# Optimization experiments

Hardware: AMD Instinct MI355X
Metric: run time of the kernel (lower is better)

Reference implementation:

```python
import jax, jax.numpy as jnp
import numpy as np

B, S, H, U = 32, 2048, 1024, 1024


def setup_inputs() -> dict:
    key = jax.random.key(0)
    ks = jax.random.split(key, 5)
    sc = 1.0 / np.sqrt(H)
    return {
        "hidden_t": jax.random.normal(ks[0], (B, H), jnp.float32),
        "hiddens": jax.random.normal(ks[1], (B, S, H), jnp.float32),
        "W1": jax.random.normal(ks[2], (H, U), jnp.float32) * sc,
        "b1": jnp.zeros((U,), jnp.float32),
        "W2": jax.random.normal(ks[3], (H, U), jnp.float32) * sc,
        "b2": jnp.zeros((U,), jnp.float32),
        "V": jax.random.normal(ks[4], (U, 1), jnp.float32) * sc,
        "bV": jnp.zeros((1,), jnp.float32),
    }


def reference(hidden_t, hiddens, W1, b1, W2, b2, V, bV):
    # proj of encoder states: [B,S,U]; proj of decoder state broadcast over time: [B,1,U]
    keys = jnp.einsum("bsh,hu->bsu", hiddens, W1) + b1
    query = (hidden_t @ W2 + b2)[:, None, :]
    score = jnp.tanh(keys + query) @ V + bV            # [B,S,1]
    attention_weights = jax.nn.softmax(score, axis=1)  # softmax over seq axis
    context_vector = jnp.sum(attention_weights * hiddens, axis=1)  # [B,H]
    return context_vector, attention_weights
```

## Files before the change

### kernel.cpp

```cpp
#include <hip/hip_runtime.h>
#include <hip/hip_bf16.h>
#include <cstdint>

#define S_LEN 2048
#define B_SZ  32
#define H_DIM 1024
#define U_DIM 1024

#define BM 128
#define BN 128
#define BK 64

using short8  = __attribute__((ext_vector_type(8))) short;
using floatx4 = __attribute__((ext_vector_type(4))) float;

typedef __attribute__((address_space(3))) void lds_void;
typedef const __attribute__((address_space(1))) void glb_void;
#define GLD16(g, s) __builtin_amdgcn_global_load_lds((glb_void*)(g), (lds_void*)(s), 16, 0, 0)

__device__ __forceinline__ unsigned short f32_to_bf16_rne(float f) {
    unsigned int u = __float_as_uint(f);
    unsigned int r = (u + 0x7fffu + ((u >> 16) & 1u)) >> 16;
    return (unsigned short)r;
}

__global__ __launch_bounds__(256)
void cast_hiddens_kernel(const float* __restrict__ src, unsigned short* __restrict__ dst) {
    const size_t i = ((size_t)blockIdx.x * 256 + threadIdx.x) * 8;
    float4 a = *(const float4*)(src + i);
    float4 b = *(const float4*)(src + i + 4);
    ushort4 lo, hi;
    lo.x = f32_to_bf16_rne(a.x); lo.y = f32_to_bf16_rne(a.y);
    lo.z = f32_to_bf16_rne(a.z); lo.w = f32_to_bf16_rne(a.w);
    hi.x = f32_to_bf16_rne(b.x); hi.y = f32_to_bf16_rne(b.y);
    hi.z = f32_to_bf16_rne(b.z); hi.w = f32_to_bf16_rne(b.w);
    *(ushort4*)(dst + i)     = lo;
    *(ushort4*)(dst + i + 4) = hi;
}

__global__ void transpose_cast_w1(const float* __restrict__ W1,
                                  unsigned short* __restrict__ W1t) {
    __shared__ float tile[32][33];
    const int tx = threadIdx.x, ty = threadIdx.y;
    const int u0 = blockIdx.x * 32, h0 = blockIdx.y * 32;
#pragma unroll
    for (int i = 0; i < 4; ++i)
        tile[ty * 4 + i][tx] = W1[(size_t)(h0 + ty * 4 + i) * U_DIM + u0 + tx];
    __syncthreads();
#pragma unroll
    for (int i = 0; i < 4; ++i)
        W1t[(size_t)(u0 + ty * 4 + i) * H_DIM + h0 + tx] =
            f32_to_bf16_rne(tile[tx][ty * 4 + i]);
}

__global__ __launch_bounds__(128)
void query_kernel_v2(const float* __restrict__ hidden_t,
                     const float* __restrict__ W2,
                     const float* __restrict__ b1,
                     const float* __restrict__ b2,
                     float* __restrict__ query) {
    const int b  = blockIdx.z;
    const int hc = blockIdx.y;
    const int u  = blockIdx.x * 128 + threadIdx.x;
    const float* ht = hidden_t + b * H_DIM + hc * 128;
    const float* w  = W2 + (size_t)hc * 128 * U_DIM + u;
    float acc = (hc == 0) ? (b1[u] + b2[u]) : 0.f;
#pragma unroll 8
    for (int h = 0; h < 128; ++h)
        acc = fmaf(ht[h], w[(size_t)h * U_DIM], acc);
    atomicAdd(&query[b * U_DIM + u], acc);
}

__device__ __forceinline__ void score_epilogue(const floatx4 acc[4][4],
                                               const float* __restrict__ qrow,
                                               const float* __restrict__ V,
                                               float* __restrict__ scores,
                                               int m0, int n0, int wr, int wc, int q, int r) {
#pragma unroll
    for (int mt = 0; mt < 4; ++mt) {
#pragma unroll
        for (int reg = 0; reg < 4; ++reg) {
            float sum = 0.f;
#pragma unroll
            for (int nt = 0; nt < 4; ++nt) {
                const int c = n0 + wc * 64 + nt * 16 + r;
                float x = acc[mt][nt][reg] + qrow[c];
                x = fminf(fmaxf(x, -15.f), 15.f);
                float e = __expf(2.f * x);
                float t = (e - 1.f) / (e + 1.f);
                sum = fmaf(t, V[c], sum);
            }
            sum += __shfl_xor(sum, 1);
            sum += __shfl_xor(sum, 2);
            sum += __shfl_xor(sum, 4);
            sum += __shfl_xor(sum, 8);
            if (r == 0)
                atomicAdd(&scores[m0 + wr * 64 + mt * 16 + q * 4 + reg], sum);
        }
    }
}

__global__ __launch_bounds__(256)
void keys_score_v4(const unsigned short* __restrict__ hb,
                   const unsigned short* __restrict__ W1t,
                   const float* __restrict__ query,
                   const float* __restrict__ V,
                   float* __restrict__ scores) {
    __shared__ unsigned short As[BM * BK];
    __shared__ unsigned short Bs[BN * BK];

    const int tid = threadIdx.x;
    const int w = tid >> 6, l = tid & 63;
    const int q = l >> 4, r = l & 15;
    const int wr = w >> 1, wc = w & 1;

    const int bid = blockIdx.x;
    const int col      = (bid >> 3) & 7;
    const int row_band = ((bid >> 6) << 3) | (bid & 7);
    const int m0 = row_band * BM;
    const int n0 = col * BN;

    const int srow   = l >> 3;
    const int gchunk = ((l & 7) ^ srow) * 8;

    const unsigned short* gA = hb  + ((size_t)(m0 + w * 8 + srow) << 10) + gchunk;
    const unsigned short* gB = W1t + ((size_t)(n0 + w * 8 + srow) << 10) + gchunk;
    unsigned short* lA = &As[(w * 8) * BK];
    unsigned short* lB = &Bs[(w * 8) * BK];

    floatx4 acc[4][4];
#pragma unroll
    for (int mt = 0; mt < 4; ++mt)
#pragma unroll
        for (int nt = 0; nt < 4; ++nt)
            acc[mt][nt] = (floatx4){0.f, 0.f, 0.f, 0.f};

    const int r7 = r & 7;
    for (int kt = 0; kt < H_DIM / BK; ++kt) {
#pragma unroll
        for (int i = 0; i < 4; ++i) {
            GLD16(gA + ((size_t)(i * 32) << 10), lA + i * 32 * BK);
            GLD16(gB + ((size_t)(i * 32) << 10), lB + i * 32 * BK);
        }
        gA += BK; gB += BK;

        __syncthreads();

#pragma unroll
        for (int kh = 0; kh < 2; ++kh) {
            short8 af[4], bfr[4];
#pragma unroll
            for (int mt = 0; mt < 4; ++mt)
                af[mt] = *(const short8*)
                    &As[(wr * 64 + mt * 16 + r) * BK + (((kh << 2) | q) ^ r7) * 8];
#pragma unroll
            for (int nt = 0; nt < 4; ++nt)
                bfr[nt] = *(const short8*)
                    &Bs[(wc * 64 + nt * 16 + r) * BK + (((kh << 2) | q) ^ r7) * 8];
#pragma unroll
            for (int mt = 0; mt < 4; ++mt)
#pragma unroll
                for (int nt = 0; nt < 4; ++nt)
                    acc[mt][nt] = __builtin_amdgcn_mfma_f32_16x16x32_bf16(
                        af[mt], bfr[nt], acc[mt][nt], 0, 0, 0);
        }

        __syncthreads();
    }

    const float* qrow = query + (m0 >> 11) * U_DIM;
    score_epilogue(acc, qrow, V, scores, m0, n0, wr, wc, q, r);
}

__global__ __launch_bounds__(256)
void keys_score_v1(const float* __restrict__ hiddens,
                   const unsigned short* __restrict__ W1t,
                   const float* __restrict__ query,
                   const float* __restrict__ V,
                   float* __restrict__ scores) {
    __shared__ unsigned short As[BM][40];
    __shared__ unsigned short Bs[BN][40];
    const int tid = threadIdx.x;
    const int lane = tid & 63, wave = tid >> 6;
    const int q = lane >> 4, r = lane & 15;
    const int wr = wave >> 1, wc = wave & 1;
    const int m0 = blockIdx.y * BM, n0 = blockIdx.x * BN;
    const int arow = tid >> 3, achunk = tid & 7;
    const int brow = tid >> 2, bchunk = tid & 3;
    floatx4 acc[4][4];
#pragma unroll
    for (int mt = 0; mt < 4; ++mt)
#pragma unroll
        for (int nt = 0; nt < 4; ++nt)
            acc[mt][nt] = (floatx4){0.f, 0.f, 0.f, 0.f};
    for (int kt = 0; kt < H_DIM / 32; ++kt) {
        const float* ag = hiddens + (size_t)(m0 + arow) * H_DIM + kt * 32 + achunk * 4;
#pragma unroll
        for (int i = 0; i < 4; ++i) {
            float4 f = *(const float4*)(ag + (size_t)i * 32 * H_DIM);
            ushort4 h;
            h.x = f32_to_bf16_rne(f.x); h.y = f32_to_bf16_rne(f.y);
            h.z = f32_to_bf16_rne(f.z); h.w = f32_to_bf16_rne(f.w);
            *(ushort4*)&As[arow + i * 32][achunk * 4] = h;
        }
        const unsigned short* bg = W1t + (size_t)(n0 + brow) * H_DIM + kt * 32 + bchunk * 8;
#pragma unroll
        for (int i = 0; i < 2; ++i)
            *(uint4*)&Bs[brow + i * 64][bchunk * 8] = *(const uint4*)(bg + (size_t)i * 64 * H_DIM);
        __syncthreads();
        short8 af[4], bfr[4];
#pragma unroll
        for (int mt = 0; mt < 4; ++mt)
            af[mt] = *(const short8*)&As[wr * 64 + mt * 16 + r][q * 8];
#pragma unroll
        for (int nt = 0; nt < 4; ++nt)
            bfr[nt] = *(const short8*)&Bs[wc * 64 + nt * 16 + r][q * 8];
#pragma unroll
        for (int mt = 0; mt < 4; ++mt)
#pragma unroll
            for (int nt = 0; nt < 4; ++nt)
                acc[mt][nt] = __builtin_amdgcn_mfma_f32_16x16x32_bf16(
                    af[mt], bfr[nt], acc[mt][nt], 0, 0, 0);
        __syncthreads();
    }
    const float* qrow = query + (m0 >> 11) * U_DIM;
    score_epilogue(acc, qrow, V, scores, m0, n0, wr, wc, q, r);
}

__global__ __launch_bounds__(256)
void softmax_stats_kernel(const float* __restrict__ scores,
                          float2* __restrict__ stats) {
    const int b = blockIdx.x, tid = threadIdx.x;
    const int wave = tid >> 6, lane = tid & 63;
    const float* src = scores + b * S_LEN;
    float v[8];
    float m = -1e30f;
#pragma unroll
    for (int i = 0; i < 8; ++i) { v[i] = src[tid + i * 256]; m = fmaxf(m, v[i]); }
#pragma unroll
    for (int off = 32; off >= 1; off >>= 1) m = fmaxf(m, __shfl_xor(m, off));
    __shared__ float red[4];
    if (lane == 0) red[wave] = m;
    __syncthreads();
    m = fmaxf(fmaxf(red[0], red[1]), fmaxf(red[2], red[3]));
    __syncthreads();
    float s = 0.f;
#pragma unroll
    for (int i = 0; i < 8; ++i) s += __expf(v[i] - m);
#pragma unroll
    for (int off = 32; off >= 1; off >>= 1) s += __shfl_xor(s, off);
    if (lane == 0) red[wave] = s;
    __syncthreads();
    if (tid == 0) {
        s = red[0] + red[1] + red[2] + red[3];
        stats[b] = make_float2(m, 1.f / s);
    }
}

__global__ __launch_bounds__(256)
void context_partial_kernel(const float* __restrict__ scores,
                            const float2* __restrict__ stats,
                            const float* __restrict__ hiddens,
                            float* __restrict__ out_w,
                            float* __restrict__ partial) {
    const int b = blockIdx.y, sc = blockIdx.x;
    const int tid = threadIdx.x;
    __shared__ float wsm[128];

    const float2 st = stats[b];
    if (tid < 128) {
        const int s = sc * 128 + tid;
        const float w = __expf(scores[b * S_LEN + s] - st.x) * st.y;
        wsm[tid] = w;
        out_w[b * S_LEN + s] = w;
    }
    __syncthreads();

    const float* hbase = hiddens + ((size_t)b * S_LEN + sc * 128) * H_DIM + tid * 4;
    float4 acc = make_float4(0.f, 0.f, 0.f, 0.f);
#pragma unroll 4
    for (int s = 0; s < 128; ++s) {
        const float w = wsm[s];
        float4 hv = *(const float4*)(hbase + (size_t)s * H_DIM);
        acc.x = fmaf(w, hv.x, acc.x);
        acc.y = fmaf(w, hv.y, acc.y);
        acc.z = fmaf(w, hv.z, acc.z);
        acc.w = fmaf(w, hv.w, acc.w);
    }
    *(float4*)(partial + ((size_t)(b * 16 + sc) << 10) + tid * 4) = acc;
}

__global__ __launch_bounds__(256)
void context_reduce_kernel(const float* __restrict__ partial,
                           float* __restrict__ out_ctx) {
    const int b = blockIdx.x, tid = threadIdx.x;
    float4 acc = make_float4(0.f, 0.f, 0.f, 0.f);
#pragma unroll
    for (int sc = 0; sc < 16; ++sc) {
        float4 p = *(const float4*)(partial + ((size_t)(b * 16 + sc) << 10) + tid * 4);
        acc.x += p.x; acc.y += p.y; acc.z += p.z; acc.w += p.w;
    }
    *(float4*)(out_ctx + b * H_DIM + tid * 4) = acc;
}

extern "C" void kernel_launch(void* const* d_in, const int* in_sizes, int n_in,
                              void* d_out, int out_size, void* d_ws, size_t ws_size,
                              hipStream_t stream) {
    const float* hidden_t = (const float*)d_in[0];
    const float* hiddens  = (const float*)d_in[1];
    const float* W1       = (const float*)d_in[2];
    const float* b1       = (const float*)d_in[3];
    const float* W2       = (const float*)d_in[4];
    const float* b2       = (const float*)d_in[5];
    const float* V        = (const float*)d_in[6];

    float* out_ctx = (float*)d_out;
    float* out_w   = (float*)d_out + B_SZ * H_DIM;

    char* ws = (char*)d_ws;
    unsigned short* W1t = (unsigned short*)ws;
    float*  query   = (float*)(ws + (2u << 20));
    float*  scores  = query + B_SZ * U_DIM;
    float2* stats   = (float2*)(scores + B_SZ * S_LEN);
    float*  partial = (float*)(ws + (3u << 20));
    unsigned short* hb = (unsigned short*)(ws + (6u << 20));
    const size_t need = (6u << 20) + (size_t)B_SZ * S_LEN * H_DIM * 2;

    hipMemsetAsync(query,  0, (size_t)B_SZ * U_DIM * sizeof(float), stream);
    hipMemsetAsync(scores, 0, (size_t)B_SZ * S_LEN * sizeof(float), stream);

    transpose_cast_w1<<<dim3(32, 32), dim3(32, 8), 0, stream>>>(W1, W1t);
    query_kernel_v2<<<dim3(8, 8, B_SZ), 128, 0, stream>>>(hidden_t, W2, b1, b2, query);

    if (ws_size >= need) {
        cast_hiddens_kernel<<<32768, 256, 0, stream>>>(hiddens, hb);
        keys_score_v4<<<(U_DIM / BN) * ((B_SZ * S_LEN) / BM), 256, 0, stream>>>(
            hb, W1t, query, V, scores);
    } else {
        keys_score_v1<<<dim3(U_DIM / 128, (B_SZ * S_LEN) / BM), 256, 0, stream>>>(
            hiddens, W1t, query, V, scores);
    }

    softmax_stats_kernel<<<B_SZ, 256, 0, stream>>>(scores, stats);
    context_partial_kernel<<<dim3(16, B_SZ), 256, 0, stream>>>(
        scores, stats, hiddens, out_w, partial);
    context_reduce_kernel<<<B_SZ, 256, 0, stream>>>(partial, out_ctx);
}
```

Measured before the change: 648.2 us.

## Replace keys GEMM with 256x256 double-buffered 8-wave pipelined MFMA kernel

Swaps the 128x128 single-buffered keys/score GEMM for a 256x256 tile kernel with 512 threads. It double-buffers LDS and staggers the global-to-LDS loads of A and B across phases so they overlap the MFMA work, and raises wave priority during the MFMA bursts. The larger tile cuts global traffic per FLOP. In exchange it uses 128KB of LDS per block, limiting occupancy to one block per CU, and relies on hand-placed waitcnt and barrier sequencing that is fragile.

Result: no change. 635.6 us (-2.0%).

```diff
diff --git a/kernel.cpp b/kernel.cpp
--- a/kernel.cpp
+++ b/kernel.cpp
@@ -6,10 +6,6 @@
 #define B_SZ  32
 #define H_DIM 1024
 #define U_DIM 1024
-
-#define BM 128
-#define BN 128
-#define BK 64
 
 using short8  = __attribute__((ext_vector_type(8))) short;
 using floatx4 = __attribute__((ext_vector_type(4))) float;
@@ -71,24 +67,223 @@
     atomicAdd(&query[b * U_DIM + u], acc);
 }
 
-__device__ __forceinline__ void score_epilogue(const floatx4 acc[4][4],
-                                               const float* __restrict__ qrow,
-                                               const float* __restrict__ V,
-                                               float* __restrict__ scores,
-                                               int m0, int n0, int wr, int wc, int q, int r) {
-#pragma unroll
-    for (int mt = 0; mt < 4; ++mt) {
+__global__ __launch_bounds__(512)
+void keys_score_v5(const unsigned short* __restrict__ hb,
+                   const unsigned short* __restrict__ W1t,
+                   const float* __restrict__ query,
+                   const float* __restrict__ V,
+                   float* __restrict__ scores) {
+    __shared__ unsigned short As[2][256 * 64];
+    __shared__ unsigned short Bs[2][256 * 64];
+
+    const int tid = threadIdx.x;
+    const int w = tid >> 6, l = tid & 63;
+    const int q = l >> 4, r = l & 15, r7 = l & 7;
+    const int wr = w >> 2, wc = w & 3;
+
+    const int bid = blockIdx.x;
+    const int wg  = (bid & 7) * 128 + (bid >> 3);
+    const int m0 = (wg >> 2) << 8;
+    const int n0 = (wg & 3) << 8;
+
+    const int srow = l >> 3;
+    const int gch  = ((l & 7) ^ srow) << 3;
+
+    const unsigned short* gA = hb  + ((size_t)(m0 + w * 8 + srow) << 10) + gch;
+    const unsigned short* gB = W1t + ((size_t)(n0 + w * 8 + srow) << 10) + gch;
+    const int wbase = (w * 8) << 6;
+
+    floatx4 acc[8][4];
+#pragma unroll
+    for (int mt = 0; mt < 8; ++mt)
+#pragma unroll
+        for (int nt = 0; nt < 4; ++nt)
+            acc[mt][nt] = (floatx4){0.f, 0.f, 0.f, 0.f};
+
+#define STAGE_A(t, d)                                                         \
+    {                                                                         \
+        const unsigned short* _g = gA + ((size_t)(t) << 6);                   \
+        _Pragma("unroll")                                                     \
+        for (int _i = 0; _i < 4; ++_i)                                        \
+            GLD16(_g + ((size_t)(_i * 64) << 10), &As[d][wbase + _i * 4096]); \
+    }
+#define STAGE_B(t, d)                                                         \
+    {                                                                         \
+        const unsigned short* _g = gB + ((size_t)(t) << 6);                   \
+        _Pragma("unroll")                                                     \
+        for (int _i = 0; _i < 4; ++_i)                                        \
+            GLD16(_g + ((size_t)(_i * 64) << 10), &Bs[d][wbase + _i * 4096]); \
+    }
+
+    const int arow0 = (wr * 128 + r) << 6;
+    const int brow0 = (wc * 64 + r) << 6;
+    const int ch0 = (q ^ r7) << 3;
+    const int ch1 = ((4 | q) ^ r7) << 3;
+
+    STAGE_A(0, 0); STAGE_B(0, 0); STAGE_A(1, 1);
+    asm volatile("s_waitcnt vmcnt(4)" ::: "memory");
+    __builtin_amdgcn_s_barrier();
+
+    for (int kt = 0; kt < 16; ++kt) {
+        const int c = kt & 1, nc = c ^ 1;
+        const int tB = (kt + 1 < 16) ? kt + 1 : 15;
+        const int tA = (kt + 2 < 16) ? kt + 2 : 15;
+        short8 af[8], b0, b1;
+
+#pragma unroll
+        for (int mt = 0; mt < 8; ++mt)
+            af[mt] = *(const short8*)&As[c][arow0 + mt * 1024 + ch0];
+        b0 = *(const short8*)&Bs[c][brow0 + ch0];
+        b1 = *(const short8*)&Bs[c][brow0 + 1024 + ch0];
+        STAGE_B(tB, nc);
+        __builtin_amdgcn_s_barrier();
+        asm volatile("s_waitcnt lgkmcnt(0)" ::: "memory");
+        __builtin_amdgcn_s_setprio(1);
+#pragma unroll
+        for (int mt = 0; mt < 8; ++mt) {
+            acc[mt][0] = __builtin_amdgcn_mfma_f32_16x16x32_bf16(af[mt], b0, acc[mt][0], 0, 0, 0);
+            acc[mt][1] = __builtin_amdgcn_mfma_f32_16x16x32_bf16(af[mt], b1, acc[mt][1], 0, 0, 0);
+        }
+        __builtin_amdgcn_s_setprio(0);
+        __builtin_amdgcn_s_barrier();
+
+        b0 = *(const short8*)&Bs[c][brow0 + 2048 + ch0];
+        b1 = *(const short8*)&Bs[c][brow0 + 3072 + ch0];
+        __builtin_amdgcn_s_barrier();
+        asm volatile("s_waitcnt lgkmcnt(0)" ::: "memory");
+        __builtin_amdgcn_s_setprio(1);
+#pragma unroll
+        for (int mt = 0; mt < 8; ++mt) {
+            acc[mt][2] = __builtin_amdgcn_mfma_f32_16x16x32_bf16(af[mt], b0, acc[mt][2], 0, 0, 0);
+            acc[mt][3] = __builtin_amdgcn_mfma_f32_16x16x32_bf16(af[mt], b1, acc[mt][3], 0, 0, 0);
+        }
+        __builtin_amdgcn_s_setprio(0);
+        __builtin_amdgcn_s_barrier();
+
+#pragma unroll
+        for (int mt = 0; mt < 8; ++mt)
+            af[mt] = *(const short8*)&As[c][arow0 + mt * 1024 + ch1];
+        b0 = *(const short8*)&Bs[c][brow0 + ch1];
+        b1 = *(const short8*)&Bs[c][brow0 + 1024 + ch1];
+        __builtin_amdgcn_s_barrier();
+        asm volatile("s_waitcnt lgkmcnt(0)" ::: "memory");
+        __builtin_amdgcn_s_setprio(1);
+#pragma unroll
+        for (int mt = 0; mt < 8; ++mt) {
+            acc[mt][0] = __builtin_amdgcn_mfma_f32_16x16x32_bf16(af[mt], b0, acc[mt][0], 0, 0, 0);
+            acc[mt][1] = __builtin_amdgcn_mfma_f32_16x16x32_bf16(af[mt], b1, acc[mt][1], 0, 0, 0);
+        }
+        __builtin_amdgcn_s_setprio(0);
+        __builtin_amdgcn_s_barrier();
+
+        b0 = *(const short8*)&Bs[c][brow0 + 2048 + ch1];
+        b1 = *(const short8*)&Bs[c][brow0 + 3072 + ch1];
+        STAGE_A(tA, c);
+        asm volatile("s_waitcnt vmcnt(4)" ::: "memory");
+        __builtin_amdgcn_s_barrier();
+        asm volatile("s_waitcnt lgkmcnt(0)" ::: "memory");
+        __builtin_amdgcn_s_setprio(1);
+#pragma unroll
+        for (int mt = 0; mt < 8; ++mt) {
+            acc[mt][2] = __builtin_amdgcn_mfma_f32_16x16x32_bf16(af[mt], b0, acc[mt][2], 0, 0, 0);
+            acc[mt][3] = __builtin_amdgcn_mfma_f32_16x16x32_bf16(af[mt], b1, acc[mt][3], 0, 0, 0);
+        }
+        __builtin_amdgcn_s_setprio(0);
+        __builtin_amdgcn_s_barrier();
+    }
+#undef STAGE_A
+#undef STAGE_B
+
+    const float* qrow = query + (m0 >> 11) * U_DIM;
+#pragma unroll
+    for (int mt = 0; mt < 8; ++mt) {
 #pragma unroll
         for (int reg = 0; reg < 4; ++reg) {
             float sum = 0.f;
 #pragma unroll
             for (int nt = 0; nt < 4; ++nt) {
-                const int c = n0 + wc * 64 + nt * 16 + r;
-                float x = acc[mt][nt][reg] + qrow[c];
+                const int cc = n0 + wc * 64 + nt * 16 + r;
+                float x = acc[mt][nt][reg] + qrow[cc];
                 x = fminf(fmaxf(x, -15.f), 15.f);
                 float e = __expf(2.f * x);
                 float t = (e - 1.f) / (e + 1.f);
-                sum = fmaf(t, V[c], sum);
+                sum = fmaf(t, V[cc], sum);
+            }
+            sum += __shfl_xor(sum, 1);
+            sum += __shfl_xor(sum, 2);
+            sum += __shfl_xor(sum, 4);
+            sum += __shfl_xor(sum, 8);
+            if (r == 0)
+                atomicAdd(&scores[m0 + wr * 128 + mt * 16 + q * 4 + reg], sum);
+        }
+    }
+}
+
+__global__ __launch_bounds__(256)
+void keys_score_v1(const float* __restrict__ hiddens,
+                   const unsigned short* __restrict__ W1t,
+                   const float* __restrict__ query,
+                   const float* __restrict__ V,
+                   float* __restrict__ scores) {
+    __shared__ unsigned short As[128][40];
+    __shared__ unsigned short Bs[128][40];
+    const int tid = threadIdx.x;
+    const int lane = tid & 63, wave = tid >> 6;
+    const int q = lane >> 4, r = lane & 15;
+    const int wr = wave >> 1, wc = wave & 1;
+    const int m0 = blockIdx.y * 128, n0 = blockIdx.x * 128;
+    const int arow = tid >> 3, achunk = tid & 7;
+    const int brow = tid >> 2, bchunk = tid & 3;
+    floatx4 acc[4][4];
+#pragma unroll
+    for (int mt = 0; mt < 4; ++mt)
+#pragma unroll
+        for (int nt = 0; nt < 4; ++nt)
+            acc[mt][nt] = (floatx4){0.f, 0.f, 0.f, 0.f};
+    for (int kt = 0; kt < H_DIM / 32; ++kt) {
+        const float* ag = hiddens + (size_t)(m0 + arow) * H_DIM + kt * 32 + achunk * 4;
+#pragma unroll
+        for (int i = 0; i < 4; ++i) {
+            float4 f = *(const float4*)(ag + (size_t)i * 32 * H_DIM);
+            ushort4 h;
+            h.x = f32_to_bf16_rne(f.x); h.y = f32_to_bf16_rne(f.y);
+            h.z = f32_to_bf16_rne(f.z); h.w = f32_to_bf16_rne(f.w);
+            *(ushort4*)&As[arow + i * 32][achunk * 4] = h;
+        }
+        const unsigned short* bg = W1t + (size_t)(n0 + brow) * H_DIM + kt * 32 + bchunk * 8;
+#pragma unroll
+        for (int i = 0; i < 2; ++i)
+            *(uint4*)&Bs[brow + i * 64][bchunk * 8] = *(const uint4*)(bg + (size_t)i * 64 * H_DIM);
+        __syncthreads();
+        short8 af[4], bfr[4];
+#pragma unroll
+        for (int mt = 0; mt < 4; ++mt)
+            af[mt] = *(const short8*)&As[wr * 64 + mt * 16 + r][q * 8];
+#pragma unroll
+        for (int nt = 0; nt < 4; ++nt)
+            bfr[nt] = *(const short8*)&Bs[wc * 64 + nt * 16 + r][q * 8];
+#pragma unroll
+        for (int mt = 0; mt < 4; ++mt)
+#pragma unroll
+            for (int nt = 0; nt < 4; ++nt)
+                acc[mt][nt] = __builtin_amdgcn_mfma_f32_16x16x32_bf16(
+                    af[mt], bfr[nt], acc[mt][nt], 0, 0, 0);
+        __syncthreads();
+    }
+    const float* qrow = query + (m0 >> 11) * U_DIM;
+#pragma unroll
+    for (int mt = 0; mt < 4; ++mt) {
+#pragma unroll
+        for (int reg = 0; reg < 4; ++reg) {
+            float sum = 0.f;
+#pragma unroll
+            for (int nt = 0; nt < 4; ++nt) {
+                const int cc = n0 + wc * 64 + nt * 16 + r;
+                float x = acc[mt][nt][reg] + qrow[cc];
+                x = fminf(fmaxf(x, -15.f), 15.f);
+                float e = __expf(2.f * x);
+                float t = (e - 1.f) / (e + 1.f);
+                sum = fmaf(t, V[cc], sum);
             }
             sum += __shfl_xor(sum, 1);
             sum += __shfl_xor(sum, 2);
@@ -98,133 +293,6 @@
                 atomicAdd(&scores[m0 + wr * 64 + mt * 16 + q * 4 + reg], sum);
         }
     }
-}
-
-__global__ __launch_bounds__(256)
-void keys_score_v4(const unsigned short* __restrict__ hb,
-                   const unsigned short* __restrict__ W1t,
-                   const float* __restrict__ query,
-                   const float* __restrict__ V,
-                   float* __restrict__ scores) {
-    __shared__ unsigned short As[BM * BK];
-    __shared__ unsigned short Bs[BN * BK];
-
-    const int tid = threadIdx.x;
-    const int w = tid >> 6, l = tid & 63;
-    const int q = l >> 4, r = l & 15;
-    const int wr = w >> 1, wc = w & 1;
-
-    const int bid = blockIdx.x;
-    const int col      = (bid >> 3) & 7;
-    const int row_band = ((bid >> 6) << 3) | (bid & 7);
-    const int m0 = row_band * BM;
-    const int n0 = col * BN;
-
-    const int srow   = l >> 3;
-    const int gchunk = ((l & 7) ^ srow) * 8;
-
-    const unsigned short* gA = hb  + ((size_t)(m0 + w * 8 + srow) << 10) + gchunk;
-    const unsigned short* gB = W1t + ((size_t)(n0 + w * 8 + srow) << 10) + gchunk;
-    unsigned short* lA = &As[(w * 8) * BK];
-    unsigned short* lB = &Bs[(w * 8) * BK];
-
-    floatx4 acc[4][4];
-#pragma unroll
-    for (int mt = 0; mt < 4; ++mt)
-#pragma unroll
-        for (int nt = 0; nt < 4; ++nt)
-            acc[mt][nt] = (floatx4){0.f, 0.f, 0.f, 0.f};
-
-    const int r7 = r & 7;
-    for (int kt = 0; kt < H_DIM / BK; ++kt) {
-#pragma unroll
-        for (int i = 0; i < 4; ++i) {
-            GLD16(gA + ((size_t)(i * 32) << 10), lA + i * 32 * BK);
-            GLD16(gB + ((size_t)(i * 32) << 10), lB + i * 32 * BK);
-        }
-        gA += BK; gB += BK;
-
-        __syncthreads();
-
-#pragma unroll
-        for (int kh = 0; kh < 2; ++kh) {
-            short8 af[4], bfr[4];
-#pragma unroll
-            for (int mt = 0; mt < 4; ++mt)
-                af[mt] = *(const short8*)
-                    &As[(wr * 64 + mt * 16 + r) * BK + (((kh << 2) | q) ^ r7) * 8];
-#pragma unroll
-            for (int nt = 0; nt < 4; ++nt)
-                bfr[nt] = *(const short8*)
-                    &Bs[(wc * 64 + nt * 16 + r) * BK + (((kh << 2) | q) ^ r7) * 8];
-#pragma unroll
-            for (int mt = 0; mt < 4; ++mt)
-#pragma unroll
-                for (int nt = 0; nt < 4; ++nt)
-                    acc[mt][nt] = __builtin_amdgcn_mfma_f32_16x16x32_bf16(
-                        af[mt], bfr[nt], acc[mt][nt], 0, 0, 0);
-        }
-
-        __syncthreads();
-    }
-
-    const float* qrow = query + (m0 >> 11) * U_DIM;
-    score_epilogue(acc, qrow, V, scores, m0, n0, wr, wc, q, r);
-}
-
-__global__ __launch_bounds__(256)
-void keys_score_v1(const float* __restrict__ hiddens,
-                   const unsigned short* __restrict__ W1t,
-                   const float* __restrict__ query,
-                   const float* __restrict__ V,
-                   float* __restrict__ scores) {
-    __shared__ unsigned short As[BM][40];
-    __shared__ unsigned short Bs[BN][40];
-    const int tid = threadIdx.x;
-    const int lane = tid & 63, wave = tid >> 6;
-    const int q = lane >> 4, r = lane & 15;
-    const int wr = wave >> 1, wc = wave & 1;
-    const int m0 = blockIdx.y * BM, n0 = blockIdx.x * BN;
-    const int arow = tid >> 3, achunk = tid & 7;
-    const int brow = tid >> 2, bchunk = tid & 3;
-    floatx4 acc[4][4];
-#pragma unroll
-    for (int mt = 0; mt < 4; ++mt)
-#pragma unroll
-        for (int nt = 0; nt < 4; ++nt)
-            acc[mt][nt] = (floatx4){0.f, 0.f, 0.f, 0.f};
-    for (int kt = 0; kt < H_DIM / 32; ++kt) {
-        const float* ag = hiddens + (size_t)(m0 + arow) * H_DIM + kt * 32 + achunk * 4;
-#pragma unroll
-        for (int i = 0; i < 4; ++i) {
-            float4 f = *(const float4*)(ag + (size_t)i * 32 * H_DIM);
-            ushort4 h;
-            h.x = f32_to_bf16_rne(f.x); h.y = f32_to_bf16_rne(f.y);
-            h.z = f32_to_bf16_rne(f.z); h.w = f32_to_bf16_rne(f.w);
-            *(ushort4*)&As[arow + i * 32][achunk * 4] = h;
-        }
-        const unsigned short* bg = W1t + (size_t)(n0 + brow) * H_DIM + kt * 32 + bchunk * 8;
-#pragma unroll
-        for (int i = 0; i < 2; ++i)
-            *(uint4*)&Bs[brow + i * 64][bchunk * 8] = *(const uint4*)(bg + (size_t)i * 64 * H_DIM);
-        __syncthreads();
-        short8 af[4], bfr[4];
-#pragma unroll
-        for (int mt = 0; mt < 4; ++mt)
-            af[mt] = *(const short8*)&As[wr * 64 + mt * 16 + r][q * 8];
-#pragma unroll
-        for (int nt = 0; nt < 4; ++nt)
-            bfr[nt] = *(const short8*)&Bs[wc * 64 + nt * 16 + r][q * 8];
-#pragma unroll
-        for (int mt = 0; mt < 4; ++mt)
-#pragma unroll
-            for (int nt = 0; nt < 4; ++nt)
-                acc[mt][nt] = __builtin_amdgcn_mfma_f32_16x16x32_bf16(
-                    af[mt], bfr[nt], acc[mt][nt], 0, 0, 0);
-        __syncthreads();
-    }
-    const float* qrow = query + (m0 >> 11) * U_DIM;
-    score_epilogue(acc, qrow, V, scores, m0, n0, wr, wc, q, r);
 }
 
 __global__ __launch_bounds__(256)
@@ -334,10 +402,10 @@
 
     if (ws_size >= need) {
         cast_hiddens_kernel<<<32768, 256, 0, stream>>>(hiddens, hb);
-        keys_score_v4<<<(U_DIM / BN) * ((B_SZ * S_LEN) / BM), 256, 0, stream>>>(
+        keys_score_v5<<<(B_SZ * S_LEN / 256) * (U_DIM / 256), 512, 0, stream>>>(
             hb, W1t, query, V, scores);
     } else {
-        keys_score_v1<<<dim3(U_DIM / 128, (B_SZ * S_LEN) / BM), 256, 0, stream>>>(
+        keys_score_v1<<<dim3(U_DIM / 128, (B_SZ * S_LEN) / 128), 256, 0, stream>>>(
             hiddens, W1t, query, V, scores);
     }
 
```

## Fuse hiddens bf16 cast into double-buffered pipelined keys/score GEMM

Applied to the files above, without the earlier changes.

Removes the separate cast_hiddens pass and the bf16 copy of hiddens in workspace. The GEMM kernel now loads fp32 hiddens through registers, converts them to bf16 in-kernel and writes to LDS. It double-buffers LDS, prefetches A two tiles ahead and B one tile ahead, and uses explicit waitcnt, sched barriers and setprio around the MFMAs. It also remaps blocks so consecutive blocks share column tiles, and uses an rcp-based tanh without clamping. The aim is to avoid writing and re-reading a 128MB bf16 intermediate, at the cost of higher register and LDS pressure and fragile manual synchronisation.

Result: slower. 753.3 us (+16.2%).

```diff
diff --git a/kernel.cpp b/kernel.cpp
--- a/kernel.cpp
+++ b/kernel.cpp
@@ -7,11 +7,8 @@
 #define H_DIM 1024
 #define U_DIM 1024
 
-#define BM 128
-#define BN 128
-#define BK 64
-
 using short8  = __attribute__((ext_vector_type(8))) short;
+using ushort8 = __attribute__((ext_vector_type(8))) unsigned short;
 using floatx4 = __attribute__((ext_vector_type(4))) float;
 
 typedef __attribute__((address_space(3))) void lds_void;
@@ -24,18 +21,9 @@
     return (unsigned short)r;
 }
 
-__global__ __launch_bounds__(256)
-void cast_hiddens_kernel(const float* __restrict__ src, unsigned short* __restrict__ dst) {
-    const size_t i = ((size_t)blockIdx.x * 256 + threadIdx.x) * 8;
-    float4 a = *(const float4*)(src + i);
-    float4 b = *(const float4*)(src + i + 4);
-    ushort4 lo, hi;
-    lo.x = f32_to_bf16_rne(a.x); lo.y = f32_to_bf16_rne(a.y);
-    lo.z = f32_to_bf16_rne(a.z); lo.w = f32_to_bf16_rne(a.w);
-    hi.x = f32_to_bf16_rne(b.x); hi.y = f32_to_bf16_rne(b.y);
-    hi.z = f32_to_bf16_rne(b.z); hi.w = f32_to_bf16_rne(b.w);
-    *(ushort4*)(dst + i)     = lo;
-    *(ushort4*)(dst + i + 4) = hi;
+__device__ __forceinline__ float fast_tanh(float x) {
+    float e = __expf(2.f * x);
+    return 1.f - 2.f * __builtin_amdgcn_rcpf(e + 1.f);
 }
 
 __global__ void transpose_cast_w1(const float* __restrict__ W1,
@@ -71,11 +59,143 @@
     atomicAdd(&query[b * U_DIM + u], acc);
 }
 
-__device__ __forceinline__ void score_epilogue(const floatx4 acc[4][4],
-                                               const float* __restrict__ qrow,
-                                               const float* __restrict__ V,
-                                               float* __restrict__ scores,
-                                               int m0, int n0, int wr, int wc, int q, int r) {
+__global__ __launch_bounds__(256, 2)
+void keys_score_v7(const float* __restrict__ hiddens,
+                   const unsigned short* __restrict__ W1t,
+                   const float* __restrict__ query,
+                   const float* __restrict__ V,
+                   float* __restrict__ scores) {
+    __shared__ unsigned short As[2][128 * 64];
+    __shared__ unsigned short Bs[2][128 * 64];
+
+    const int tid = threadIdx.x;
+    const int w = tid >> 6, l = tid & 63;
+    const int q = l >> 4, r = l & 15, r7 = l & 7;
+    const int wr = w >> 1, wc = w & 1;
+
+    const int bid = blockIdx.x;
+    const int wg  = (bid & 7) * 512 + (bid >> 3);
+    const int m0 = (wg >> 3) << 7;
+    const int n0 = (wg & 7) << 7;
+
+    const int arow  = tid >> 1;
+    const int ahalf = tid & 1;
+    const int ar7   = arow & 7;
+    const float* gAf = hiddens + (size_t)(m0 + arow) * H_DIM + ahalf * 32;
+    const int awrow = arow << 6;
+
+    const int srow = l >> 3;
+    const int gch  = ((l & 7) ^ srow) << 3;
+    const unsigned short* gB = W1t + ((size_t)(n0 + w * 32 + srow) << 10) + gch;
+    const int bwbase = (w * 32) << 6;
+
+    floatx4 acc[4][4];
+#pragma unroll
+    for (int mt = 0; mt < 4; ++mt)
+#pragma unroll
+        for (int nt = 0; nt < 4; ++nt)
+            acc[mt][nt] = (floatx4){0.f, 0.f, 0.f, 0.f};
+
+#define LOADA(t, ra)                                                          \
+    {                                                                         \
+        const float* _g = gAf + ((t) << 6);                                   \
+        _Pragma("unroll")                                                     \
+        for (int _j = 0; _j < 8; ++_j)                                        \
+            ra[_j] = *(const float4*)(_g + _j * 4);                           \
+    }
+#define WRITEA(d, ra)                                                         \
+    {                                                                         \
+        _Pragma("unroll")                                                     \
+        for (int _c = 0; _c < 4; ++_c) {                                      \
+            ushort8 _pk;                                                      \
+            _pk[0] = f32_to_bf16_rne(ra[2 * _c].x);                           \
+            _pk[1] = f32_to_bf16_rne(ra[2 * _c].y);                           \
+            _pk[2] = f32_to_bf16_rne(ra[2 * _c].z);                           \
+            _pk[3] = f32_to_bf16_rne(ra[2 * _c].w);                           \
+            _pk[4] = f32_to_bf16_rne(ra[2 * _c + 1].x);                       \
+            _pk[5] = f32_to_bf16_rne(ra[2 * _c + 1].y);                       \
+            _pk[6] = f32_to_bf16_rne(ra[2 * _c + 1].z);                       \
+            _pk[7] = f32_to_bf16_rne(ra[2 * _c + 1].w);                       \
+            *(ushort8*)&As[d][awrow + (((ahalf * 4 + _c) ^ ar7) << 3)] = _pk; \
+        }                                                                     \
+    }
+#define STAGE_B(t, d)                                                         \
+    {                                                                         \
+        const unsigned short* _g = gB + ((size_t)(t) << 6);                   \
+        _Pragma("unroll")                                                     \
+        for (int _i = 0; _i < 4; ++_i)                                        \
+            GLD16(_g + ((size_t)(_i * 8) << 10), &Bs[d][bwbase + _i * 512]);  \
+    }
+
+    float4 raP[8], ra[8];
+
+    LOADA(0, raP);
+    STAGE_B(0, 0);
+    LOADA(1, ra);
+    asm volatile("s_waitcnt vmcnt(12)" ::: "memory");
+    __builtin_amdgcn_sched_barrier(0);
+    WRITEA(0, raP);
+    asm volatile("s_waitcnt vmcnt(8)" ::: "memory");
+    asm volatile("s_waitcnt lgkmcnt(0)" ::: "memory");
+    __builtin_amdgcn_s_barrier();
+
+    const int ch0 = (q ^ r7) << 3;
+    const int ch1 = ((4 | q) ^ r7) << 3;
+
+    for (int kt = 0; kt < 16; ++kt) {
+        const int c = kt & 1, nc = c ^ 1;
+        const int tB = (kt + 1 < 16) ? kt + 1 : 15;
+        const int tA = (kt + 2 < 16) ? kt + 2 : 15;
+
+        STAGE_B(tB, nc);
+        asm volatile("s_waitcnt vmcnt(4)" ::: "memory");
+        __builtin_amdgcn_sched_barrier(0);
+        WRITEA(nc, ra);
+        LOADA(tA, ra);
+
+        short8 af[4], bf[4];
+#pragma unroll
+        for (int mt = 0; mt < 4; ++mt)
+            af[mt] = *(const short8*)&As[c][((wr * 64 + mt * 16 + r) << 6) + ch0];
+#pragma unroll
+        for (int nt = 0; nt < 4; ++nt)
+            bf[nt] = *(const short8*)&Bs[c][((wc * 64 + nt * 16 + r) << 6) + ch0];
+        asm volatile("s_waitcnt lgkmcnt(0)" ::: "memory");
+        __builtin_amdgcn_sched_barrier(0);
+        __builtin_amdgcn_s_setprio(1);
+#pragma unroll
+        for (int mt = 0; mt < 4; ++mt)
+#pragma unroll
+            for (int nt = 0; nt < 4; ++nt)
+                acc[mt][nt] = __builtin_amdgcn_mfma_f32_16x16x32_bf16(
+                    af[mt], bf[nt], acc[mt][nt], 0, 0, 0);
+        __builtin_amdgcn_s_setprio(0);
+
+#pragma unroll
+        for (int mt = 0; mt < 4; ++mt)
+            af[mt] = *(const short8*)&As[c][((wr * 64 + mt * 16 + r) << 6) + ch1];
+#pragma unroll
+        for (int nt = 0; nt < 4; ++nt)
+            bf[nt] = *(const short8*)&Bs[c][((wc * 64 + nt * 16 + r) << 6) + ch1];
+        asm volatile("s_waitcnt lgkmcnt(0)" ::: "memory");
+        __builtin_amdgcn_sched_barrier(0);
+        __builtin_amdgcn_s_setprio(1);
+#pragma unroll
+        for (int mt = 0; mt < 4; ++mt)
+#pragma unroll
+            for (int nt = 0; nt < 4; ++nt)
+                acc[mt][nt] = __builtin_amdgcn_mfma_f32_16x16x32_bf16(
+                    af[mt], bf[nt], acc[mt][nt], 0, 0, 0);
+        __builtin_amdgcn_s_setprio(0);
+
+        asm volatile("s_waitcnt vmcnt(8)" ::: "memory");
+        __builtin_amdgcn_s_barrier();
+    }
+#undef LOADA
+#undef WRITEA
+#undef STAGE_B
+
+    const float* qrow = query + (m0 >> 11) * U_DIM;
 #pragma unroll
     for (int mt = 0; mt < 4; ++mt) {
 #pragma unroll
@@ -83,12 +203,9 @@
             float sum = 0.f;
 #pragma unroll
             for (int nt = 0; nt < 4; ++nt) {
-                const int c = n0 + wc * 64 + nt * 16 + r;
-                float x = acc[mt][nt][reg] + qrow[c];
-                x = fminf(fmaxf(x, -15.f), 15.f);
-                float e = __expf(2.f * x);
-                float t = (e - 1.f) / (e + 1.f);
-                sum = fmaf(t, V[c], sum);
+                const int cc = n0 + wc * 64 + nt * 16 + r;
+                float t = fast_tanh(acc[mt][nt][reg] + qrow[cc]);
+                sum = fmaf(t, V[cc], sum);
             }
             sum += __shfl_xor(sum, 1);
             sum += __shfl_xor(sum, 2);
@@ -98,133 +215,6 @@
                 atomicAdd(&scores[m0 + wr * 64 + mt * 16 + q * 4 + reg], sum);
         }
     }
-}
-
-__global__ __launch_bounds__(256)
-void keys_score_v4(const unsigned short* __restrict__ hb,
-                   const unsigned short* __restrict__ W1t,
-                   const float* __restrict__ query,
-                   const float* __restrict__ V,
-                   float* __restrict__ scores) {
-    __shared__ unsigned short As[BM * BK];
-    __shared__ unsigned short Bs[BN * BK];
-
-    const int tid = threadIdx.x;
-    const int w = tid >> 6, l = tid & 63;
-    const int q = l >> 4, r = l & 15;
-    const int wr = w >> 1, wc = w & 1;
-
-    const int bid = blockIdx.x;
-    const int col      = (bid >> 3) & 7;
-    const int row_band = ((bid >> 6) << 3) | (bid & 7);
-    const int m0 = row_band * BM;
-    const int n0 = col * BN;
-
-    const int srow   = l >> 3;
-    const int gchunk = ((l & 7) ^ srow) * 8;
-
-    const unsigned short* gA = hb  + ((size_t)(m0 + w * 8 + srow) << 10) + gchunk;
-    const unsigned short* gB = W1t + ((size_t)(n0 + w * 8 + srow) << 10) + gchunk;
-    unsigned short* lA = &As[(w * 8) * BK];
-    unsigned short* lB = &Bs[(w * 8) * BK];
-
-    floatx4 acc[4][4];
-#pragma unroll
-    for (int mt = 0; mt < 4; ++mt)
-#pragma unroll
-        for (int nt = 0; nt < 4; ++nt)
-            acc[mt][nt] = (floatx4){0.f, 0.f, 0.f, 0.f};
-
-    const int r7 = r & 7;
-    for (int kt = 0; kt < H_DIM / BK; ++kt) {
-#pragma unroll
-        for (int i = 0; i < 4; ++i) {
-            GLD16(gA + ((size_t)(i * 32) << 10), lA + i * 32 * BK);
-            GLD16(gB + ((size_t)(i * 32) << 10), lB + i * 32 * BK);
-        }
-        gA += BK; gB += BK;
-
-        __syncthreads();
-
-#pragma unroll
-        for (int kh = 0; kh < 2; ++kh) {
-            short8 af[4], bfr[4];
-#pragma unroll
-            for (int mt = 0; mt < 4; ++mt)
-                af[mt] = *(const short8*)
-                    &As[(wr * 64 + mt * 16 + r) * BK + (((kh << 2) | q) ^ r7) * 8];
-#pragma unroll
-            for (int nt = 0; nt < 4; ++nt)
-                bfr[nt] = *(const short8*)
-                    &Bs[(wc * 64 + nt * 16 + r) * BK + (((kh << 2) | q) ^ r7) * 8];
-#pragma unroll
-            for (int mt = 0; mt < 4; ++mt)
-#pragma unroll
-                for (int nt = 0; nt < 4; ++nt)
-                    acc[mt][nt] = __builtin_amdgcn_mfma_f32_16x16x32_bf16(
-                        af[mt], bfr[nt], acc[mt][nt], 0, 0, 0);
-        }
-
-        __syncthreads();
-    }
-
-    const float* qrow = query + (m0 >> 11) * U_DIM;
-    score_epilogue(acc, qrow, V, scores, m0, n0, wr, wc, q, r);
-}
-
-__global__ __launch_bounds__(256)
-void keys_score_v1(const float* __restrict__ hiddens,
-                   const unsigned short* __restrict__ W1t,
-                   const float* __restrict__ query,
-                   const float* __restrict__ V,
-                   float* __restrict__ scores) {
-    __shared__ unsigned short As[BM][40];
-    __shared__ unsigned short Bs[BN][40];
-    const int tid = threadIdx.x;
-    const int lane = tid & 63, wave = tid >> 6;
-    const int q = lane >> 4, r = lane & 15;
-    const int wr = wave >> 1, wc = wave & 1;
-    const int m0 = blockIdx.y * BM, n0 = blockIdx.x * BN;
-    const int arow = tid >> 3, achunk = tid & 7;
-    const int brow = tid >> 2, bchunk = tid & 3;
-    floatx4 acc[4][4];
-#pragma unroll
-    for (int mt = 0; mt < 4; ++mt)
-#pragma unroll
-        for (int nt = 0; nt < 4; ++nt)
-            acc[mt][nt] = (floatx4){0.f, 0.f, 0.f, 0.f};
-    for (int kt = 0; kt < H_DIM / 32; ++kt) {
-        const float* ag = hiddens + (size_t)(m0 + arow) * H_DIM + kt * 32 + achunk * 4;
-#pragma unroll
-        for (int i = 0; i < 4; ++i) {
-            float4 f = *(const float4*)(ag + (size_t)i * 32 * H_DIM);
-            ushort4 h;
-            h.x = f32_to_bf16_rne(f.x); h.y = f32_to_bf16_rne(f.y);
-            h.z = f32_to_bf16_rne(f.z); h.w = f32_to_bf16_rne(f.w);
-            *(ushort4*)&As[arow + i * 32][achunk * 4] = h;
-        }
-        const unsigned short* bg = W1t + (size_t)(n0 + brow) * H_DIM + kt * 32 + bchunk * 8;
-#pragma unroll
-        for (int i = 0; i < 2; ++i)
-            *(uint4*)&Bs[brow + i * 64][bchunk * 8] = *(const uint4*)(bg + (size_t)i * 64 * H_DIM);
-        __syncthreads();
-        short8 af[4], bfr[4];
-#pragma unroll
-        for (int mt = 0; mt < 4; ++mt)
-            af[mt] = *(const short8*)&As[wr * 64 + mt * 16 + r][q * 8];
-#pragma unroll
-        for (int nt = 0; nt < 4; ++nt)
-            bfr[nt] = *(const short8*)&Bs[wc * 64 + nt * 16 + r][q * 8];
-#pragma unroll
-        for (int mt = 0; mt < 4; ++mt)
-#pragma unroll
-            for (int nt = 0; nt < 4; ++nt)
-                acc[mt][nt] = __builtin_amdgcn_mfma_f32_16x16x32_bf16(
-                    af[mt], bfr[nt], acc[mt][nt], 0, 0, 0);
-        __syncthreads();
-    }
-    const float* qrow = query + (m0 >> 11) * U_DIM;
-    score_epilogue(acc, qrow, V, scores, m0, n0, wr, wc, q, r);
 }
 
 __global__ __launch_bounds__(256)
@@ -323,8 +313,6 @@
     float*  scores  = query + B_SZ * U_DIM;
     float2* stats   = (float2*)(scores + B_SZ * S_LEN);
     float*  partial = (float*)(ws + (3u << 20));
-    unsigned short* hb = (unsigned short*)(ws + (6u << 20));
-    const size_t need = (6u << 20) + (size_t)B_SZ * S_LEN * H_DIM * 2;
 
     hipMemsetAsync(query,  0, (size_t)B_SZ * U_DIM * sizeof(float), stream);
     hipMemsetAsync(scores, 0, (size_t)B_SZ * S_LEN * sizeof(float), stream);
@@ -332,14 +320,7 @@
     transpose_cast_w1<<<dim3(32, 32), dim3(32, 8), 0, stream>>>(W1, W1t);
     query_kernel_v2<<<dim3(8, 8, B_SZ), 128, 0, stream>>>(hidden_t, W2, b1, b2, query);
 
-    if (ws_size >= need) {
-        cast_hiddens_kernel<<<32768, 256, 0, stream>>>(hiddens, hb);
-        keys_score_v4<<<(U_DIM / BN) * ((B_SZ * S_LEN) / BM), 256, 0, stream>>>(
-            hb, W1t, query, V, scores);
-    } else {
-        keys_score_v1<<<dim3(U_DIM / 128, (B_SZ * S_LEN) / BM), 256, 0, stream>>>(
-            hiddens, W1t, query, V, scores);
-    }
+    keys_score_v7<<<4096, 256, 0, stream>>>(hiddens, W1t, query, V, scores);
 
     softmax_stats_kernel<<<B_SZ, 256, 0, stream>>>(scores, stats);
     context_partial_kernel<<<dim3(16, B_SZ), 256, 0, stream>>>(
```
